# Optimization experiments

Measured on AMD Instinct MI355X. Metric: run time of the kernel, lower is better.

The kernel has to match this reference:

```python
import jax, jax.numpy as jnp
import numpy as np

D_MODEL = 1024
NUM_HEADS = 16
GROUP_SIZE = 4
NUM_GROUPS = NUM_HEADS // GROUP_SIZE  # 4
D_K = D_MODEL // NUM_HEADS            # 64
THETA = 10000.0
WINDOW = 512


def _rope(x, positions):
    # x: (..., t, d) with d even; interleaved-pair rotation, freq_i = theta^{-i/(d/2)}
    d = x.shape[-1]
    half = d // 2
    inv_freq = THETA ** (-jnp.arange(half, dtype=x.dtype) / half)          # (half,)
    ang = positions.astype(x.dtype)[:, None] * inv_freq[None, :]           # (t, half)
    cos, sin = jnp.cos(ang), jnp.sin(ang)
    x1, x2 = x[..., 0::2], x[..., 1::2]
    r1 = x1 * cos - x2 * sin
    r2 = x1 * sin + x2 * cos
    return jnp.stack([r1, r2], axis=-1).reshape(x.shape)


def setup_inputs() -> dict:
    key = jax.random.key(0)
    k1, k2, k3, k4, k5 = jax.random.split(key, 5)
    b, t = 2, 2048
    scale = 1.0 / np.sqrt(D_MODEL)
    return {
        "x": jax.random.normal(k1, (b, t, D_MODEL), dtype=jnp.float32),
        "WQ": jax.random.normal(k2, (D_MODEL, D_MODEL), dtype=jnp.float32) * scale,
        "WK": jax.random.normal(k3, (NUM_GROUPS * D_K, D_MODEL), dtype=jnp.float32) * scale,
        "WV": jax.random.normal(k4, (NUM_GROUPS * D_K, D_MODEL), dtype=jnp.float32) * scale,
        "WO": jax.random.normal(k5, (D_MODEL, D_MODEL), dtype=jnp.float32) * scale,
        "token_positions": jnp.arange(t, dtype=jnp.int32),
    }


def reference(x, WQ, WK, WV, WO, token_positions):
    b, t, _ = x.shape
    g, s, d = NUM_GROUPS, GROUP_SIZE, D_K
    # projections (Linear: y = x @ W^T, no bias)
    q = (x @ WQ.T).reshape(b, t, g, s, d).transpose(0, 2, 3, 1, 4)  # b g s t d
    k = (x @ WK.T).reshape(b, t, g, d).transpose(0, 2, 1, 3)        # b g t d
    v = (x @ WV.T).reshape(b, t, g, d).transpose(0, 2, 1, 3)        # b g t d
    q = _rope(q, token_positions)
    k = _rope(k, token_positions)
    # scores: kv heads shared across the s query heads of each group
    scores = jnp.einsum('bgsqd,bgkd->bgsqk', q, k) / jnp.sqrt(jnp.asarray(d, x.dtype))
    i = jnp.arange(t)[:, None]
    j = jnp.arange(t)[None, :]
    allowed = (i >= j) & (i - j <= WINDOW)  # causal sliding window
    scores = jnp.where(allowed, scores, -jnp.inf)
    probs = jax.nn.softmax(scores, axis=-1)
    out = jnp.einsum('bgsqk,bgkd->bgsqd', probs, v)                 # b g s t d
    out = out.transpose(0, 3, 1, 2, 4).reshape(b, t, D_MODEL)       # b t (g s d)
    return out @ WO.T
```

## Files before the change

kernel.cpp:

```cpp
#include <hip/hip_runtime.h>
#include <hip/hip_bf16.h>

typedef __bf16 bf16;
typedef __bf16 bf16x8 __attribute__((ext_vector_type(8)));
typedef float  floatx4 __attribute__((ext_vector_type(4)));

#define D_MODEL   1024
#define NUM_HEADS 16
#define NUM_GROUPS 4
#define DK        64
#define SEQ_T     2048
#define BATCH     2
#define M_ROWS    (BATCH*SEQ_T)
#define WINDOW    512
#define KV_DIM    (NUM_GROUPS*DK)
#define N_QKV     (D_MODEL + 2*KV_DIM)
#define QSCALE    0.1803368801111204f
#define FREQ_C    0.4152410118609203f

#define GLDS16(g, l)                                                          \
    __builtin_amdgcn_global_load_lds(                                         \
        (const __attribute__((address_space(1))) void*)(g),                   \
        (__attribute__((address_space(3))) void*)(l), 16, 0, 0)

__global__ __launch_bounds__(256)
void convert_all(const float* s0, bf16* d0, int c0,
                 const float* s1, bf16* d1, int c1,
                 const float* s2, bf16* d2, int c2,
                 const float* s3, bf16* d3, int c3,
                 const float* s4, bf16* d4, int c4)
{
    int id = blockIdx.x * 256 + threadIdx.x;
    const float* src; bf16* dst;
    if      (id < c0)         { src = s0; dst = d0; }
    else if ((id -= c0) < c1) { src = s1; dst = d1; }
    else if ((id -= c1) < c2) { src = s2; dst = d2; }
    else if ((id -= c2) < c3) { src = s3; dst = d3; }
    else if ((id -= c3) < c4) { src = s4; dst = d4; }
    else return;
    int i = id * 8;
    const float* s = src + i;
    float4 a = *(const float4*)s;
    float4 b = *(const float4*)(s + 4);
    bf16x8 v;
    v[0] = (bf16)a.x; v[1] = (bf16)a.y; v[2] = (bf16)a.z; v[3] = (bf16)a.w;
    v[4] = (bf16)b.x; v[5] = (bf16)b.y; v[6] = (bf16)b.z; v[7] = (bf16)b.w;
    *(bf16x8*)&dst[i] = v;
}

__global__ __launch_bounds__(256)
void gemm64(const bf16* __restrict__ A, const bf16* __restrict__ W, int K,
            bf16* __restrict__ Cq, bf16* __restrict__ Ck, bf16* __restrict__ Cv,
            float* __restrict__ Co, const int* __restrict__ pos, int mode, int N)
{
    __shared__ bf16 As0[64 * 32], As1[64 * 32];
    __shared__ bf16 Bs0[128 * 32], Bs1[128 * 32];

    const int tid  = threadIdx.x;
    const int wave = tid >> 6;
    const int lane = tid & 63;
    const int lr   = lane & 15;
    const int quad = lane >> 4;
    const int m0 = blockIdx.y * 64;
    const int n0 = blockIdx.x * 128;
    const int wm = (wave >> 1) * 32;
    const int wn = (wave & 1) * 64;

    const int srow = (lane >> 2);
    const int scol = (lane & 3) * 8;
    const bf16* Ap  = &A[(size_t)(m0 + wave * 16 + srow) * K + scol];
    const bf16* Wp0 = &W[(size_t)(n0 + wave * 16 + srow) * K + scol];
    const bf16* Wp1 = &W[(size_t)(n0 + 64 + wave * 16 + srow) * K + scol];
    bf16* As0d  = &As0[wave * 512];
    bf16* As1d  = &As1[wave * 512];
    bf16* Bs0d0 = &Bs0[wave * 512];
    bf16* Bs0d1 = &Bs0[(wave + 4) * 512];
    bf16* Bs1d0 = &Bs1[wave * 512];
    bf16* Bs1d1 = &Bs1[(wave + 4) * 512];

    floatx4 acc[2][4];
#pragma unroll
    for (int i = 0; i < 2; i++)
#pragma unroll
        for (int j = 0; j < 4; j++) acc[i][j] = (floatx4)(0.0f);

    for (int k0 = 0; k0 < K; k0 += 64) {
        __syncthreads();
        GLDS16(Ap + k0,       As0d);
        GLDS16(Ap + k0 + 32,  As1d);
        GLDS16(Wp0 + k0,      Bs0d0);
        GLDS16(Wp1 + k0,      Bs0d1);
        GLDS16(Wp0 + k0 + 32, Bs1d0);
        GLDS16(Wp1 + k0 + 32, Bs1d1);
        __syncthreads();

        bf16x8 a0[2], a1[2], b0[4], b1[4];
#pragma unroll
        for (int mi = 0; mi < 2; mi++) {
            a0[mi] = *(const bf16x8*)&As0[(wm + mi * 16 + lr) * 32 + quad * 8];
            a1[mi] = *(const bf16x8*)&As1[(wm + mi * 16 + lr) * 32 + quad * 8];
        }
#pragma unroll
        for (int ni = 0; ni < 4; ni++) {
            b0[ni] = *(const bf16x8*)&Bs0[(wn + ni * 16 + lr) * 32 + quad * 8];
            b1[ni] = *(const bf16x8*)&Bs1[(wn + ni * 16 + lr) * 32 + quad * 8];
        }

#pragma unroll
        for (int mi = 0; mi < 2; mi++)
#pragma unroll
            for (int ni = 0; ni < 4; ni++) {
                acc[mi][ni] = __builtin_amdgcn_mfma_f32_16x16x32_bf16(
                    a0[mi], b0[ni], acc[mi][ni], 0, 0, 0);
                acc[mi][ni] = __builtin_amdgcn_mfma_f32_16x16x32_bf16(
                    a1[mi], b1[ni], acc[mi][ni], 0, 0, 0);
            }
    }

    if (mode == 0) {
        bf16* out; int ld, coff;
        if (n0 < D_MODEL)               { out = Cq; ld = D_MODEL; coff = n0; }
        else if (n0 < D_MODEL + KV_DIM) { out = Ck; ld = KV_DIM;  coff = n0 - D_MODEL; }
        else                            { out = Cv; ld = KV_DIM;  coff = n0 - D_MODEL - KV_DIM; }
        const bool rope = (n0 < D_MODEL + KV_DIM);
        const float sc  = (n0 < D_MODEL) ? QSCALE : 1.0f;
        float inv[4];
        float sgn = (lr & 1) ? 1.0f : -1.0f;
        if (rope) {
#pragma unroll
            for (int ni = 0; ni < 4; ni++) {
                int ip = (ni * 16 + lr) >> 1;
                inv[ni] = exp2f(-(float)ip * FREQ_C);
            }
        }
#pragma unroll
        for (int mi = 0; mi < 2; mi++) {
#pragma unroll
            for (int r = 0; r < 4; r++) {
                int row = m0 + wm + mi * 16 + quad * 4 + r;
                float p = rope ? (float)pos[row & (SEQ_T - 1)] : 0.0f;
#pragma unroll
                for (int ni = 0; ni < 4; ni++) {
                    float v = acc[mi][ni][r];
                    if (rope) {
                        float vp = __shfl_xor(v, 1);
                        float ang = p * inv[ni];
                        float ss, cc;
                        __sincosf(ang, &ss, &cc);
                        v = v * cc + vp * ss * sgn;
                    }
                    out[(size_t)row * ld + coff + wn + ni * 16 + lr] = (bf16)(v * sc);
                }
            }
        }
    } else {
#pragma unroll
        for (int mi = 0; mi < 2; mi++)
#pragma unroll
            for (int ni = 0; ni < 4; ni++)
#pragma unroll
                for (int r = 0; r < 4; r++) {
                    int row = m0 + wm + mi * 16 + quad * 4 + r;
                    int col = n0 + wn + ni * 16 + lr;
                    Co[(size_t)row * N + col] = acc[mi][ni][r];
                }
    }
}

__global__ __launch_bounds__(256)
void transpose_v(const bf16* __restrict__ Vw, bf16* __restrict__ Vt)
{
    __shared__ bf16 Ts[64 * 72];
    const int tid = threadIdx.x;
    const int bg = blockIdx.x >> 5;
    const int tt = blockIdx.x & 31;
    const int b = bg >> 2, g = bg & 3;
    const int t0 = tt * 64;

#pragma unroll
    for (int i = 0; i < 2; i++) {
        int c = tid + i * 256;
        int trow = c >> 3, col8 = (c & 7) * 8;
        *(bf16x8*)&Ts[trow * 72 + col8] =
            *(const bf16x8*)&Vw[(size_t)(b * SEQ_T + t0 + trow) * KV_DIM + g * 64 + col8];
    }
    __syncthreads();
#pragma unroll
    for (int i = 0; i < 2; i++) {
        int c = tid + i * 256;
        int drow = c >> 3, tcol8 = (c & 7) * 8;
        bf16x8 v;
#pragma unroll
        for (int j = 0; j < 8; j++) v[j] = Ts[(tcol8 + j) * 72 + drow];
        *(bf16x8*)&Vt[((size_t)(bg * 64 + drow)) * SEQ_T + t0 + tcol8] = v;
    }
}

__global__ __launch_bounds__(256)
void attn_mfma(const bf16* __restrict__ Q, const bf16* __restrict__ K,
               const bf16* __restrict__ Vt_g, bf16* __restrict__ AO)
{
    const int ST = 72;
    __shared__ bf16 Qs[64 * ST];
    __shared__ bf16 Ks[64 * ST];
    __shared__ bf16 Ps[64 * ST];
    __shared__ bf16 Vt[80 * ST];

    const int tid  = threadIdx.x;
    const int wave = tid >> 6;
    const int lane = tid & 63;
    const int lr   = lane & 15;
    const int quad = lane >> 4;
    const int qt = blockIdx.x, bh = blockIdx.y;
    const int b = bh >> 4, h = bh & 15, g = h >> 2;
    const int q0 = qt * 64;
    const int wq = wave * 16;

#pragma unroll
    for (int i = 0; i < 2; i++) {
        int c = tid + i * 256;
        int row = c >> 3, col8 = (c & 7) * 8;
        *(bf16x8*)&Qs[row * ST + col8] =
            *(const bf16x8*)&Q[((size_t)(b * SEQ_T + q0 + row)) * D_MODEL + h * 64 + col8];
    }
    for (int i = tid; i < 16 * ST; i += 256) Vt[64 * ST + i] = (bf16)0.0f;
    __syncthreads();
    if (tid < 64) Vt[64 * ST + tid] = (bf16)1.0f;
    __syncthreads();

    bf16x8 qf[2];
#pragma unroll
    for (int ks = 0; ks < 2; ks++)
        qf[ks] = *(const bf16x8*)&Qs[(wq + lr) * ST + ks * 32 + quad * 8];

    floatx4 o[5];
#pragma unroll
    for (int nt = 0; nt < 5; nt++) o[nt] = (floatx4)(0.0f);

    const int t0 = (q0 >= WINDOW) ? (q0 - WINDOW) : 0;

    for (int j0 = t0; j0 <= q0; j0 += 64) {
        const bool mC = (j0 == q0);
        const bool mW = (q0 >= WINDOW) && (j0 == t0);
        __syncthreads();
#pragma unroll
        for (int i = 0; i < 2; i++) {
            int c = tid + i * 256;
            int row = c >> 3, col8 = (c & 7) * 8;
            *(bf16x8*)&Ks[row * ST + col8] =
                *(const bf16x8*)&K[((size_t)(b * SEQ_T + j0 + row)) * KV_DIM + g * 64 + col8];
            *(bf16x8*)&Vt[row * ST + col8] =
                *(const bf16x8*)&Vt_g[((size_t)((b * NUM_GROUPS + g) * 64 + row)) * SEQ_T + j0 + col8];
        }
        __syncthreads();

        floatx4 s[4];
#pragma unroll
        for (int nt = 0; nt < 4; nt++) s[nt] = (floatx4)(0.0f);
#pragma unroll
        for (int ks = 0; ks < 2; ks++) {
#pragma unroll
            for (int nt = 0; nt < 4; nt++) {
                bf16x8 kf = *(const bf16x8*)&Ks[(nt * 16 + lr) * ST + ks * 32 + quad * 8];
                s[nt] = __builtin_amdgcn_mfma_f32_16x16x32_bf16(qf[ks], kf, s[nt], 0, 0, 0);
            }
        }

        if (mC) {
#pragma unroll
            for (int nt = 0; nt < 4; nt++) {
                int key = j0 + nt * 16 + lr;
#pragma unroll
                for (int r = 0; r < 4; r++) {
                    int qi_ = q0 + wq + quad * 4 + r;
                    s[nt][r] = (key <= qi_) ? s[nt][r] : -1e30f;
                }
            }
        } else if (mW) {
#pragma unroll
            for (int nt = 0; nt < 4; nt++) {
                int key = j0 + nt * 16 + lr;
#pragma unroll
                for (int r = 0; r < 4; r++) {
                    int qi_ = q0 + wq + quad * 4 + r;
                    s[nt][r] = (qi_ - key <= WINDOW) ? s[nt][r] : -1e30f;
                }
            }
        }

#pragma unroll
        for (int nt = 0; nt < 4; nt++)
#pragma unroll
            for (int r = 0; r < 4; r++)
                Ps[(wq + quad * 4 + r) * ST + nt * 16 + lr] = (bf16)exp2f(s[nt][r]);

        __asm__ volatile("s_waitcnt lgkmcnt(0)" ::: "memory");

#pragma unroll
        for (int ks = 0; ks < 2; ks++) {
            bf16x8 pf = *(const bf16x8*)&Ps[(wq + lr) * ST + ks * 32 + quad * 8];
#pragma unroll
            for (int nt = 0; nt < 5; nt++) {
                bf16x8 vf = *(const bf16x8*)&Vt[(nt * 16 + lr) * ST + ks * 32 + quad * 8];
                o[nt] = __builtin_amdgcn_mfma_f32_16x16x32_bf16(pf, vf, o[nt], 0, 0, 0);
            }
        }
    }

#pragma unroll
    for (int r = 0; r < 4; r++) {
        float l = __shfl(o[4][r], lane & 48);
        float invl = 1.0f / l;
        int row = q0 + wq + quad * 4 + r;
#pragma unroll
        for (int nt = 0; nt < 4; nt++)
            AO[((size_t)(b * SEQ_T + row)) * D_MODEL + h * 64 + nt * 16 + lr] =
                (bf16)(o[nt][r] * invl);
    }
}

extern "C" void kernel_launch(void* const* d_in, const int* in_sizes, int n_in,
                              void* d_out, int out_size, void* d_ws, size_t ws_size,
                              hipStream_t stream)
{
    const float* x  = (const float*)d_in[0];
    const float* WQ = (const float*)d_in[1];
    const float* WK = (const float*)d_in[2];
    const float* WV = (const float*)d_in[3];
    const float* WO = (const float*)d_in[4];
    const int*  pos = (const int*)d_in[5];

    char* ws   = (char*)d_ws;
    bf16* Qw   = (bf16*)ws;
    bf16* Kw   = (bf16*)(ws + (size_t) 8 * 1024 * 1024);
    bf16* Vw   = (bf16*)(ws + (size_t)10 * 1024 * 1024);
    bf16* xb   = (bf16*)(ws + (size_t)12 * 1024 * 1024);
    bf16* AO   = xb;
    bf16* Wqkv = (bf16*)(ws + (size_t)20 * 1024 * 1024);
    bf16* Vt_g = Wqkv;
    bf16* WOb  = (bf16*)(ws + (size_t)23 * 1024 * 1024);

    const int cx = (M_ROWS * D_MODEL) / 8;
    const int cq = (D_MODEL * D_MODEL) / 8;
    const int ck = (KV_DIM * D_MODEL) / 8;
    const int ctot = cx + cq + 2 * ck + cq;
    convert_all<<<ctot / 256, 256, 0, stream>>>(
        x, xb, cx,
        WQ, Wqkv, cq,
        WK, Wqkv + (size_t)D_MODEL * D_MODEL, ck,
        WV, Wqkv + (size_t)(D_MODEL + KV_DIM) * D_MODEL, ck,
        WO, WOb, cq);

    gemm64<<<dim3(N_QKV / 128, M_ROWS / 64), 256, 0, stream>>>(
        xb, Wqkv, D_MODEL, Qw, Kw, Vw, nullptr, pos, 0, N_QKV);

    transpose_v<<<256, 256, 0, stream>>>(Vw, Vt_g);

    attn_mfma<<<dim3(SEQ_T / 64, BATCH * NUM_HEADS), 256, 0, stream>>>(
        Qw, Kw, Vt_g, AO);

    gemm64<<<dim3(D_MODEL / 128, M_ROWS / 64), 256, 0, stream>>>(
        AO, WOb, D_MODEL, nullptr, nullptr, nullptr, (float*)d_out, pos, 1, D_MODEL);
}
```

Before: 156.0 us.

## Share K/V tiles across the four query heads of a GQA group per block

The attention kernel now assigns one KV group per block, with each wave handling one of its four query heads over 32 query rows. Each K and V tile loaded into shared memory is therefore reused by four heads instead of being reloaded by four separate blocks. Q fragments are read straight from global memory into registers, and the 64-key tile bounds are realigned for 32-row query tiles. The cost is half as many blocks, more registers per wave from two accumulator sets, and a larger per-wave P buffer, which could lower occupancy.

```diff
diff --git a/kernel.cpp b/kernel.cpp
--- a/kernel.cpp
+++ b/kernel.cpp
@@ -201,46 +201,45 @@
                const bf16* __restrict__ Vt_g, bf16* __restrict__ AO)
 {
     const int ST = 72;
-    __shared__ bf16 Qs[64 * ST];
     __shared__ bf16 Ks[64 * ST];
-    __shared__ bf16 Ps[64 * ST];
     __shared__ bf16 Vt[80 * ST];
+    __shared__ bf16 Ps[4 * 32 * ST];
 
     const int tid  = threadIdx.x;
     const int wave = tid >> 6;
     const int lane = tid & 63;
     const int lr   = lane & 15;
     const int quad = lane >> 4;
-    const int qt = blockIdx.x, bh = blockIdx.y;
-    const int b = bh >> 4, h = bh & 15, g = h >> 2;
-    const int q0 = qt * 64;
-    const int wq = wave * 16;
-
-#pragma unroll
-    for (int i = 0; i < 2; i++) {
-        int c = tid + i * 256;
-        int row = c >> 3, col8 = (c & 7) * 8;
-        *(bf16x8*)&Qs[row * ST + col8] =
-            *(const bf16x8*)&Q[((size_t)(b * SEQ_T + q0 + row)) * D_MODEL + h * 64 + col8];
-    }
-    for (int i = tid; i < 16 * ST; i += 256) Vt[64 * ST + i] = (bf16)0.0f;
-    __syncthreads();
-    if (tid < 64) Vt[64 * ST + tid] = (bf16)1.0f;
-    __syncthreads();
-
-    bf16x8 qf[2];
-#pragma unroll
-    for (int ks = 0; ks < 2; ks++)
-        qf[ks] = *(const bf16x8*)&Qs[(wq + lr) * ST + ks * 32 + quad * 8];
-
-    floatx4 o[5];
-#pragma unroll
-    for (int nt = 0; nt < 5; nt++) o[nt] = (floatx4)(0.0f);
-
-    const int t0 = (q0 >= WINDOW) ? (q0 - WINDOW) : 0;
-
-    for (int j0 = t0; j0 <= q0; j0 += 64) {
-        const bool mC = (j0 == q0);
+    const int bg = blockIdx.y;
+    const int b = bg >> 2, g = bg & 3;
+    const int h = g * 4 + wave;
+    const int q0 = blockIdx.x * 32;
+
+    bf16x8 qf[2][2];
+#pragma unroll
+    for (int mi = 0; mi < 2; mi++)
+#pragma unroll
+        for (int ks = 0; ks < 2; ks++)
+            qf[mi][ks] = *(const bf16x8*)
+                &Q[((size_t)(b * SEQ_T + q0 + mi * 16 + lr)) * D_MODEL
+                   + h * 64 + ks * 32 + quad * 8];
+
+    for (int i = tid; i < 15 * ST; i += 256) Vt[65 * ST + i] = (bf16)0.0f;
+    if (tid < ST) Vt[64 * ST + tid] = (bf16)(tid < 64 ? 1.0f : 0.0f);
+
+    bf16* Pw = &Ps[wave * 32 * ST];
+
+    floatx4 o[2][5];
+#pragma unroll
+    for (int mi = 0; mi < 2; mi++)
+#pragma unroll
+        for (int nt = 0; nt < 5; nt++) o[mi][nt] = (floatx4)(0.0f);
+
+    const int t0   = (q0 >= WINDOW) ? ((q0 - WINDOW) & ~63) : 0;
+    const int last = q0 & ~63;
+
+    for (int j0 = t0; j0 <= last; j0 += 64) {
+        const bool mC = (j0 == last);
         const bool mW = (q0 >= WINDOW) && (j0 == t0);
         __syncthreads();
 #pragma unroll
@@ -250,73 +249,87 @@
             *(bf16x8*)&Ks[row * ST + col8] =
                 *(const bf16x8*)&K[((size_t)(b * SEQ_T + j0 + row)) * KV_DIM + g * 64 + col8];
             *(bf16x8*)&Vt[row * ST + col8] =
-                *(const bf16x8*)&Vt_g[((size_t)((b * NUM_GROUPS + g) * 64 + row)) * SEQ_T + j0 + col8];
+                *(const bf16x8*)&Vt_g[((size_t)(bg * 64 + row)) * SEQ_T + j0 + col8];
         }
         __syncthreads();
 
-        floatx4 s[4];
-#pragma unroll
-        for (int nt = 0; nt < 4; nt++) s[nt] = (floatx4)(0.0f);
+        floatx4 s[2][4];
+#pragma unroll
+        for (int mi = 0; mi < 2; mi++)
+#pragma unroll
+            for (int nt = 0; nt < 4; nt++) s[mi][nt] = (floatx4)(0.0f);
 #pragma unroll
         for (int ks = 0; ks < 2; ks++) {
 #pragma unroll
             for (int nt = 0; nt < 4; nt++) {
                 bf16x8 kf = *(const bf16x8*)&Ks[(nt * 16 + lr) * ST + ks * 32 + quad * 8];
-                s[nt] = __builtin_amdgcn_mfma_f32_16x16x32_bf16(qf[ks], kf, s[nt], 0, 0, 0);
+                s[0][nt] = __builtin_amdgcn_mfma_f32_16x16x32_bf16(qf[0][ks], kf, s[0][nt], 0, 0, 0);
+                s[1][nt] = __builtin_amdgcn_mfma_f32_16x16x32_bf16(qf[1][ks], kf, s[1][nt], 0, 0, 0);
             }
         }
 
         if (mC) {
 #pragma unroll
-            for (int nt = 0; nt < 4; nt++) {
-                int key = j0 + nt * 16 + lr;
-#pragma unroll
-                for (int r = 0; r < 4; r++) {
-                    int qi_ = q0 + wq + quad * 4 + r;
-                    s[nt][r] = (key <= qi_) ? s[nt][r] : -1e30f;
+            for (int mi = 0; mi < 2; mi++)
+#pragma unroll
+                for (int nt = 0; nt < 4; nt++) {
+                    int key = j0 + nt * 16 + lr;
+#pragma unroll
+                    for (int r = 0; r < 4; r++) {
+                        int qi_ = q0 + mi * 16 + quad * 4 + r;
+                        s[mi][nt][r] = (key <= qi_) ? s[mi][nt][r] : -1e30f;
+                    }
                 }
-            }
         } else if (mW) {
 #pragma unroll
-            for (int nt = 0; nt < 4; nt++) {
-                int key = j0 + nt * 16 + lr;
-#pragma unroll
-                for (int r = 0; r < 4; r++) {
-                    int qi_ = q0 + wq + quad * 4 + r;
-                    s[nt][r] = (qi_ - key <= WINDOW) ? s[nt][r] : -1e30f;
+            for (int mi = 0; mi < 2; mi++)
+#pragma unroll
+                for (int nt = 0; nt < 4; nt++) {
+                    int key = j0 + nt * 16 + lr;
+#pragma unroll
+                    for (int r = 0; r < 4; r++) {
+                        int qi_ = q0 + mi * 16 + quad * 4 + r;
+                        s[mi][nt][r] = (qi_ - key <= WINDOW) ? s[mi][nt][r] : -1e30f;
+                    }
                 }
-            }
-        }
-
-#pragma unroll
-        for (int nt = 0; nt < 4; nt++)
-#pragma unroll
-            for (int r = 0; r < 4; r++)
-                Ps[(wq + quad * 4 + r) * ST + nt * 16 + lr] = (bf16)exp2f(s[nt][r]);
+        }
+
+#pragma unroll
+        for (int mi = 0; mi < 2; mi++)
+#pragma unroll
+            for (int nt = 0; nt < 4; nt++)
+#pragma unroll
+                for (int r = 0; r < 4; r++)
+                    Pw[(mi * 16 + quad * 4 + r) * ST + nt * 16 + lr] =
+                        (bf16)exp2f(s[mi][nt][r]);
 
         __asm__ volatile("s_waitcnt lgkmcnt(0)" ::: "memory");
 
 #pragma unroll
         for (int ks = 0; ks < 2; ks++) {
-            bf16x8 pf = *(const bf16x8*)&Ps[(wq + lr) * ST + ks * 32 + quad * 8];
+            bf16x8 pf0 = *(const bf16x8*)&Pw[(0 + lr) * ST + ks * 32 + quad * 8];
+            bf16x8 pf1 = *(const bf16x8*)&Pw[(16 + lr) * ST + ks * 32 + quad * 8];
 #pragma unroll
             for (int nt = 0; nt < 5; nt++) {
                 bf16x8 vf = *(const bf16x8*)&Vt[(nt * 16 + lr) * ST + ks * 32 + quad * 8];
-                o[nt] = __builtin_amdgcn_mfma_f32_16x16x32_bf16(pf, vf, o[nt], 0, 0, 0);
-            }
-        }
-    }
-
-#pragma unroll
-    for (int r = 0; r < 4; r++) {
-        float l = __shfl(o[4][r], lane & 48);
-        float invl = 1.0f / l;
-        int row = q0 + wq + quad * 4 + r;
-#pragma unroll
-        for (int nt = 0; nt < 4; nt++)
-            AO[((size_t)(b * SEQ_T + row)) * D_MODEL + h * 64 + nt * 16 + lr] =
-                (bf16)(o[nt][r] * invl);
-    }
+                o[0][nt] = __builtin_amdgcn_mfma_f32_16x16x32_bf16(pf0, vf, o[0][nt], 0, 0, 0);
+                o[1][nt] = __builtin_amdgcn_mfma_f32_16x16x32_bf16(pf1, vf, o[1][nt], 0, 0, 0);
+            }
+        }
+    }
+
+#pragma unroll
+    for (int mi = 0; mi < 2; mi++)
+#pragma unroll
+        for (int r = 0; r < 4; r++) {
+            float l = __shfl(o[mi][4][r], lane & 48);
+            float invl = 1.0f / l;
+            int row = q0 + mi * 16 + quad * 4 + r;
+#pragma unroll
+            for (int nt = 0; nt < 4; nt++)
+                AO[((size_t)(b * SEQ_T + row)) * D_MODEL + h * 64 + nt * 16 + lr] =
+                    (bf16)(o[mi][nt][r] * invl);
+        }
 }
 
 extern "C" void kernel_launch(void* const* d_in, const int* in_sizes, int n_in,
@@ -356,7 +369,7 @@
 
     transpose_v<<<256, 256, 0, stream>>>(Vw, Vt_g);
 
-    attn_mfma<<<dim3(SEQ_T / 64, BATCH * NUM_HEADS), 256, 0, stream>>>(
+    attn_mfma<<<dim3(SEQ_T / 32, BATCH * NUM_GROUPS), 256, 0, stream>>>(
         Qw, Kw, Vt_g, AO);
 
     gemm64<<<dim3(D_MODEL / 128, M_ROWS / 64), 256, 0, stream>>>(
```

After: 155.5 us. No clear change (-0.3%).
